# Performance work log

Hardware: AMD Instinct MI355X
Metric: run time of the kernel (lower is better)

Reference implementation:

```python
import jax, jax.numpy as jnp
import numpy as np

H = 16
HD = 128
ROPE_BASE = 10000.0

def _rope_cos_sin(T, dtype):
    inv_freq = 1.0 / (ROPE_BASE ** (jnp.arange(0, HD, 2, dtype=jnp.float32) / HD))  # [HD/2]
    pos = jnp.arange(T, dtype=jnp.float32)
    freqs = pos[:, None] * inv_freq[None, :]  # [T, HD/2]
    return jnp.cos(freqs).astype(dtype), jnp.sin(freqs).astype(dtype)

def _apply_rotary(x, cos, sin):
    # x: [B,H,T,HD]; cos/sin: [T,HD/2]
    x1, x2 = x[..., : HD // 2], x[..., HD // 2 :]
    c = cos[None, None, :, :]
    s = sin[None, None, :, :]
    return jnp.concatenate([x1 * c - x2 * s, x1 * s + x2 * c], axis=-1)

def setup_inputs() -> dict:
    key = jax.random.key(0)
    ks = jax.random.split(key, 5)
    B, T, D = 2, 2048, 2048
    x = jax.random.normal(ks[0], (B, T, D), dtype=jnp.float32)
    Wqkv = jax.random.normal(ks[1], (3 * D, D), dtype=jnp.float32) * (D ** -0.5)
    bqkv = jax.random.normal(ks[2], (3 * D,), dtype=jnp.float32) * 0.02
    Wo = jax.random.normal(ks[3], (D, D), dtype=jnp.float32) * (D ** -0.5)
    bo = jax.random.normal(ks[4], (D,), dtype=jnp.float32) * 0.02
    # causal mask: True = masked (future positions)
    mask = jnp.triu(jnp.ones((T, T), dtype=bool), k=1)[None, None, :, :]
    return {"x": x, "Wqkv": Wqkv, "bqkv": bqkv, "Wo": Wo, "bo": bo, "mask": mask}

def reference(x, Wqkv, bqkv, Wo, bo, mask):
    B, T, D = x.shape
    qkv = x @ Wqkv.T + bqkv  # [B,T,3D]
    q, k, v = jnp.split(qkv, 3, axis=-1)
    def to_heads(t):
        return t.reshape(B, T, H, HD).transpose(0, 2, 1, 3)  # [B,H,T,HD]
    q, k, v = to_heads(q), to_heads(k), to_heads(v)
    cos, sin = _rope_cos_sin(T, x.dtype)
    q = _apply_rotary(q, cos, sin)
    k = _apply_rotary(k, cos, sin)
    scale = HD ** 0.5
    attn = jnp.einsum('bhqd,bhkd->bhqk', q, k) / scale
    neg = -jnp.finfo(x.dtype).max
    attn = jnp.where(mask, neg, attn)
    w = jax.nn.softmax(attn, axis=-1)
    out = jnp.einsum('bhqk,bhkd->bhqd', w, v)  # [B,H,T,HD]
    out = out.transpose(0, 2, 1, 3).reshape(B, T, H * HD)
    return out @ Wo.T + bo
```

## Files before the change

### kernel.cpp

```cpp
#include <hip/hip_runtime.h>
#include <hip/hip_bf16.h>
#include <cstdint>

typedef __bf16 bf16;
typedef __bf16 bf16x8 __attribute__((ext_vector_type(8)));
typedef float  f32x4  __attribute__((ext_vector_type(4)));

#define B_   2
#define T_   2048
#define D_   2048
#define H_   16
#define HD_  128

typedef __attribute__((address_space(3))) void       lds_void;
typedef __attribute__((address_space(1))) const void gbl_void;
__device__ __forceinline__ void glds16(const bf16* g, bf16* l) {
    __builtin_amdgcn_global_load_lds((gbl_void*)g, (lds_void*)l, 16, 0, 0);
}

__device__ __forceinline__ ushort4 cvt4(const float4 v) {
    union { bf16 h[4]; ushort4 u; } pk;
    pk.h[0] = (bf16)v.x; pk.h[1] = (bf16)v.y;
    pk.h[2] = (bf16)v.z; pk.h[3] = (bf16)v.w;
    return pk.u;
}

__global__ __launch_bounds__(256) void convert_xw_kernel(
    const float* __restrict__ x, const float* __restrict__ wqkv,
    bf16* __restrict__ xb, bf16* __restrict__ wqkvb)
{
    const int NX = (B_ * T_ * D_) / 4;
    const int NT = NX + (3 * D_ * D_) / 4;
    for (int g = blockIdx.x * blockDim.x + threadIdx.x; g < NT;
         g += gridDim.x * blockDim.x) {
        if (g < NX) ((ushort4*)xb)[g]      = cvt4(((const float4*)x)[g]);
        else        ((ushort4*)wqkvb)[g-NX] = cvt4(((const float4*)wqkv)[g-NX]);
    }
}

__global__ __launch_bounds__(256) void convert_wo_kernel(
    const float* __restrict__ wo, bf16* __restrict__ wob)
{
    const int N = (D_ * D_) / 4;
    for (int g = blockIdx.x * blockDim.x + threadIdx.x; g < N;
         g += gridDim.x * blockDim.x)
        ((ushort4*)wob)[g] = cvt4(((const float4*)wo)[g]);
}

__device__ __forceinline__ void gemm_core_glds(
    const bf16* __restrict__ A, const bf16* __restrict__ W, int K,
    int bm, int bn, int tid, f32x4 (&acc)[4][4],
    bf16* lds_a, bf16* lds_b)
{
    const int lane = tid & 63, quad = lane >> 4, lcol = lane & 15;
    const int wave = tid >> 6;
    const int wm = (wave >> 1) * 64, wn2 = (wave & 1) * 32;
    const int sw = lcol & 7;
    const int sr = tid >> 3, pc = tid & 7;
    const int sc = (pc ^ (sr & 7)) * 8;
    const bf16* abase = A + (size_t)(bm * 128 + sr) * K + sc;
    const bf16* bbase = W + (size_t)(bn * 128 + sr) * K + sc;
    bf16* la = lds_a + sr * 64 + pc * 8;
    bf16* lb = lds_b + sr * 64 + pc * 8;

    for (int k0 = 0; k0 < K; k0 += 64) {
        __syncthreads();
#pragma unroll
        for (int p = 0; p < 4; p++) {
            glds16(abase + k0 + (size_t)32 * p * K, la + 2048 * p);
            glds16(bbase + k0 + (size_t)32 * p * K, lb + 2048 * p);
        }
        __syncthreads();
#pragma unroll
        for (int kk = 0; kk < 2; kk++) {
            bf16x8 af[4], bfr[4];
#pragma unroll
            for (int i = 0; i < 4; i++)
                af[i] = *(const bf16x8*)&lds_a[(wm + i * 16 + lcol) * 64 +
                                               (((kk * 4 + quad) ^ sw) * 8)];
#pragma unroll
            for (int j = 0; j < 4; j++) {
                const int row = wn2 + (j & 1) * 16 + (j >> 1) * 64 + lcol;
                bfr[j] = *(const bf16x8*)&lds_b[row * 64 +
                                                (((kk * 4 + quad) ^ sw) * 8)];
            }
#pragma unroll
            for (int i = 0; i < 4; i++)
#pragma unroll
                for (int j = 0; j < 4; j++)
                    acc[i][j] = __builtin_amdgcn_mfma_f32_16x16x32_bf16(af[i], bfr[j], acc[i][j], 0, 0, 0);
        }
    }
}

__global__ __launch_bounds__(512, 1) void qkv_gemm_kernel(
    const bf16* __restrict__ xb, const bf16* __restrict__ wqkvb,
    const float* __restrict__ bias,
    bf16* __restrict__ qh, bf16* __restrict__ kh, bf16* __restrict__ vT)
{
    __shared__ bf16 lds[8 * 8192];
    const int tid = threadIdx.x;
    const int bn = blockIdx.x, bm = blockIdx.y;
    const int lane = tid & 63, quad = lane >> 4, lcol = lane & 15;
    const int wave = tid >> 6;
    const int wm = wave >> 1;
    const int wn = wave & 1;
    const int swz = lcol & 7;

    const int sr = tid >> 3, sc = tid & 7;
    const bf16* ga = xb    + (size_t)(bm * 256 + sr) * D_ + ((sc ^ (sr & 7)) << 3);
    const bf16* gb = wqkvb + (size_t)(bn * 256 + sr) * D_ + ((sc ^ (sr & 7)) << 3);
    bf16* ldst = lds + tid * 8;

    auto stage = [&](int t, int kind) {
        const bf16* g = ((kind & 2) ? gb : ga) +
                        (size_t)(kind & 1) * 128 * D_ + t * 64;
        bf16* d = ldst + (((t & 1) * 4 + kind) & 7) * 8192;
        glds16(g, d);
        glds16(g + (size_t)64 * D_, d + 4096);
    };

    f32x4 acc[4][8];
    const f32x4 z = {0.f, 0.f, 0.f, 0.f};
#pragma unroll
    for (int i = 0; i < 4; i++)
#pragma unroll
        for (int j = 0; j < 8; j++) acc[i][j] = z;

    const int NT = D_ / 64;

    stage(0, 0); stage(0, 1); stage(0, 2); stage(0, 3);
    stage(1, 0); stage(1, 1);

#define QKV_TILE(t, par, LASTV)                                                \
    {                                                                          \
        if (LASTV) asm volatile("s_waitcnt vmcnt(0)" ::: "memory");            \
        else       asm volatile("s_waitcnt vmcnt(4)" ::: "memory");            \
        __builtin_amdgcn_s_barrier();                                          \
        __builtin_amdgcn_sched_barrier(0);                                     \
        if ((t) + 1 < NT) { stage((t) + 1, 2); stage((t) + 1, 3); }            \
        const bf16* sA = lds + ((par) + (wm >> 1)) * 8192 + ((wm & 1) * 64) * 64; \
        const bf16* sB = lds + ((par) + 2 + wn) * 8192;                        \
        bf16x8 af[4][2];                                                       \
        _Pragma("unroll")                                                      \
        for (int i = 0; i < 4; i++)                                            \
            _Pragma("unroll")                                                  \
            for (int kk = 0; kk < 2; kk++)                                     \
                af[i][kk] = *(const bf16x8*)&sA[(i * 16 + lcol) * 64 +         \
                                                (((kk * 4 + quad) ^ swz) << 3)]; \
        _Pragma("unroll")                                                      \
        for (int jp = 0; jp < 2; jp++) {                 \
            bf16x8 bf[2][2];                                                   \
            _Pragma("unroll")                                                  \
            for (int jj = 0; jj < 2; jj++)                                     \
                _Pragma("unroll")                                              \
                for (int kk = 0; kk < 2; kk++)                                 \
                    bf[jj][kk] = *(const bf16x8*)&sB[((jp * 2 + jj) * 16 + lcol) * 64 + \
                                                     (((kk * 4 + quad) ^ swz) << 3)]; \
            __builtin_amdgcn_s_setprio(1);                                     \
            _Pragma("unroll")                                                  \
            for (int jj = 0; jj < 2; jj++)                                     \
                _Pragma("unroll")                                              \
                for (int kk = 0; kk < 2; kk++)                                 \
                    _Pragma("unroll")                                          \
                    for (int i = 0; i < 4; i++)                                \
                        acc[i][jp * 2 + jj] = __builtin_amdgcn_mfma_f32_16x16x32_bf16( \
                            af[i][kk], bf[jj][kk], acc[i][jp * 2 + jj], 0, 0, 0); \
            __builtin_amdgcn_s_setprio(0);                                     \
        }                                                                      \
        __builtin_amdgcn_s_barrier();     \
        __builtin_amdgcn_sched_barrier(0);                                     \
        if ((t) + 2 < NT) { stage((t) + 2, 0); stage((t) + 2, 1); }            \
        _Pragma("unroll")                                                      \
        for (int jp = 2; jp < 4; jp++) {                 \
            bf16x8 bf[2][2];                                                   \
            _Pragma("unroll")                                                  \
            for (int jj = 0; jj < 2; jj++)                                     \
                _Pragma("unroll")                                              \
                for (int kk = 0; kk < 2; kk++)                                 \
                    bf[jj][kk] = *(const bf16x8*)&sB[((jp * 2 + jj) * 16 + lcol) * 64 + \
                                                     (((kk * 4 + quad) ^ swz) << 3)]; \
            __builtin_amdgcn_s_setprio(1);                                     \
            _Pragma("unroll")                                                  \
            for (int jj = 0; jj < 2; jj++)                                     \
                _Pragma("unroll")                                              \
                for (int kk = 0; kk < 2; kk++)                                 \
                    _Pragma("unroll")                                          \
                    for (int i = 0; i < 4; i++)                                \
                        acc[i][jp * 2 + jj] = __builtin_amdgcn_mfma_f32_16x16x32_bf16( \
                            af[i][kk], bf[jj][kk], acc[i][jp * 2 + jj], 0, 0, 0); \
            __builtin_amdgcn_s_setprio(0);                                     \
        }                                                                      \
    }

    for (int tt = 0; tt < 15; tt++) {
        QKV_TILE(2 * tt, 0, false);
        QKV_TILE(2 * tt + 1, 4, false);
    }
    QKV_TILE(30, 0, false);
    QKV_TILE(31, 4, true);
#undef QKV_TILE

    const int n0 = bn * 256 + wn * 128;
    const int part = bn >> 3;
    const int hh = (bn & 7) * 2 + wn;
    const int mb0 = bm * 256 + wm * 64;
    const int bb = mb0 >> 11, tb = mb0 & (T_ - 1);

    if (part < 2) {
        bf16* dst = (part == 0) ? qh : kh;
#pragma unroll
        for (int jp = 0; jp < 4; jp++) {
            const int d1 = jp * 16 + lcol;
            const float invf = __expf(-0.14391156831212787f * (float)d1);
            const float b1 = bias[n0 + d1];
            const float b2 = bias[n0 + d1 + 64];
#pragma unroll
            for (int i = 0; i < 4; i++) {
#pragma unroll
                for (int r = 0; r < 4; r++) {
                    const int t = tb + i * 16 + quad * 4 + r;
                    const float x1 = acc[i][jp][r] + b1;
                    const float x2 = acc[i][jp + 4][r] + b2;
                    float s, c;
                    __sincosf((float)t * invf, &s, &c);
                    const size_t rowo = ((size_t)(bb * H_ + hh) * T_ + t) * HD_;
                    dst[rowo + d1]      = (bf16)(x1 * c - x2 * s);
                    dst[rowo + d1 + 64] = (bf16)(x1 * s + x2 * c);
                }
            }
        }
    } else {
        const int bh = bb * H_ + hh;
#pragma unroll
        for (int j = 0; j < 8; j++) {
            const int d = j * 16 + lcol;
            const float bv = bias[n0 + d];
            bf16* vdst = &vT[((size_t)bh * HD_ + d) * T_ + tb];
#pragma unroll
            for (int r = 0; r < 4; r++) {
                union { bf16 hhv[4]; ushort4 u; } pk;
#pragma unroll
                for (int i = 0; i < 4; i++) pk.hhv[i] = (bf16)(acc[i][j][r] + bv);
                *(ushort4*)&vdst[(quad * 4 + r) * 4] = pk.u;
            }
        }
    }
}

__global__ __launch_bounds__(256) void attn_kernel(
    const bf16* __restrict__ qh, const bf16* __restrict__ kh,
    const bf16* __restrict__ vT, bf16* __restrict__ ctx)
{
    __shared__ bf16 lds_k[2][64 * 128];
    __shared__ bf16 lds_v[2][128 * 64];
    __shared__ bf16 lds_p[64 * 64];
    const int tid = threadIdx.x;
    const int id = blockIdx.x;
    const int bh = id & 31;
    const int qp = id >> 5;
    const int qtA = 31 - qp;
    const int qtB = qp;
    const int ktA = qtA + 1;
    const int lane = tid & 63, quad = lane >> 4, lcol = lane & 15;
    const int wave = tid >> 6;
    const int wq0 = wave * 16;
    const float scale2 = 0.08838834764831845f * 1.4426950408889634f;
    const int b = bh >> 4, h = bh & 15;

    const bf16* kbase = kh + (size_t)bh * T_ * HD_;
    const bf16* vbase = vT + (size_t)bh * HD_ * T_;

    const int ksrow = tid >> 4;
    const bf16* kstage = kbase + (size_t)ksrow * HD_ + (((tid & 15) ^ ksrow) << 3);
    const int vsd = tid >> 3;
    const bf16* vstage = vbase + (size_t)vsd * T_ + (((tid & 7) ^ (vsd & 7)) << 3);

    int qt_cur = qtA;
    int q0 = qtA * 64;

    bf16x8 qf[4];
    auto load_q = [&](int q0_) {
#pragma unroll
        for (int kk = 0; kk < 4; kk++)
            qf[kk] = *(const bf16x8*)&qh[((size_t)bh * T_ + q0_ + wq0 + lcol) * HD_ +
                                         kk * 32 + quad * 8];
    };
    load_q(q0);

    f32x4 o[8];
    const f32x4 z = {0.f, 0.f, 0.f, 0.f};
#pragma unroll
    for (int jd = 0; jd < 8; jd++) o[jd] = z;
    float l_part[4] = {0.f, 0.f, 0.f, 0.f};

    auto do_epilogue = [&](int q0_) {
        float inv_l[4];
#pragma unroll
        for (int r = 0; r < 4; r++) {
            float rs = l_part[r];
#pragma unroll
            for (int off = 1; off < 16; off <<= 1)
                rs += __shfl_xor(rs, off);
            inv_l[r] = 1.0f / rs;
        }
#pragma unroll
        for (int r = 0; r < 4; r++) {
            const int t = q0_ + wq0 + quad * 4 + r;
#pragma unroll
            for (int jd = 0; jd < 8; jd++)
                ctx[((size_t)(b * T_ + t)) * D_ + h * HD_ + jd * 16 + lcol] =
                    (bf16)(o[jd][r] * inv_l[r]);
        }
    };

#pragma unroll
    for (int p = 0; p < 4; p++) {
        glds16(kstage + (size_t)16 * p * HD_, &lds_k[0][tid * 8 + p * 2048]);
        glds16(vstage + (size_t)32 * p * T_, &lds_v[0][tid * 8 + p * 2048]);
    }

    for (int s = 0; s < 33; s++) {
        __syncthreads();
        if (s + 1 < 33) {
            const int kn = (s + 1 < ktA) ? (s + 1) : (s + 1 - ktA);
            const bf16* ks = kstage + (size_t)kn * 64 * HD_;
            const bf16* vs = vstage + kn * 64;
            bf16* lkd = &lds_k[(s + 1) & 1][tid * 8];
            bf16* lvd = &lds_v[(s + 1) & 1][tid * 8];
#pragma unroll
            for (int p = 0; p < 4; p++) {
                glds16(ks + (size_t)16 * p * HD_, lkd + p * 2048);
                glds16(vs + (size_t)32 * p * T_, lvd + p * 2048);
            }
        }
        if (s == ktA) {
            do_epilogue(q0);
            qt_cur = qtB;
            q0 = qtB * 64;
            load_q(q0);
#pragma unroll
            for (int jd = 0; jd < 8; jd++) o[jd] = z;
#pragma unroll
            for (int r = 0; r < 4; r++) l_part[r] = 0.f;
        }
        const int kt = (s < ktA) ? s : (s - ktA);
        const bf16* lk = lds_k[s & 1];
        const bf16* lv = lds_v[s & 1];

        f32x4 s_acc[4];
#pragma unroll
        for (int j = 0; j < 4; j++) s_acc[j] = z;
        __builtin_amdgcn_s_setprio(1);
#pragma unroll
        for (int kk = 0; kk < 4; kk++) {
#pragma unroll
            for (int j = 0; j < 4; j++) {
                const bf16x8 bk = *(const bf16x8*)&lk[(j * 16 + lcol) * 128 +
                                        (((kk * 4 + quad) ^ lcol) << 3)];
                s_acc[j] = __builtin_amdgcn_mfma_f32_16x16x32_bf16(qf[kk], bk, s_acc[j], 0, 0, 0);
            }
        }
        __builtin_amdgcn_s_setprio(0);

        const bool diag = (kt == qt_cur);
#pragma unroll
        for (int r = 0; r < 4; r++) {
            const int prow = wq0 + quad * 4 + r;
            const int qrow = q0 + prow;
            union { bf16 hh[4]; ushort4 u; } pk;
            float lp = 0.f;
#pragma unroll
            for (int j = 0; j < 4; j++) {
                float p = exp2f(fmaf(s_acc[j][r], scale2, -16.0f));
                if (diag) {
                    const int kcol = kt * 64 + j * 16 + lcol;
                    p = (kcol > qrow) ? 0.f : p;
                }
                lp += p;
                pk.hh[j] = (bf16)p;
            }
            l_part[r] += lp;
            *(ushort4*)&lds_p[prow * 64 + ((lcol * 4) ^ ((prow & 7) << 3))] = pk.u;
        }

#pragma unroll
        for (int kk2 = 0; kk2 < 2; kk2++) {
            const int prow = wq0 + lcol;
            const bf16x8 pf = *(const bf16x8*)&lds_p[prow * 64 +
                                  ((kk2 * 32 + quad * 8) ^ ((lcol & 7) << 3))];
            bf16x8 vf[8];
#pragma unroll
            for (int jd = 0; jd < 8; jd++) {
                const int d = jd * 16 + lcol;
                vf[jd] = *(const bf16x8*)&lv[d * 64 +
                              (((kk2 * 4 + quad) ^ (lcol & 7)) << 3)];
            }
            __builtin_amdgcn_s_setprio(1);
#pragma unroll
            for (int jd = 0; jd < 8; jd++)
                o[jd] = __builtin_amdgcn_mfma_f32_16x16x32_bf16(pf, vf[jd], o[jd], 0, 0, 0);
            __builtin_amdgcn_s_setprio(0);
        }
    }

    do_epilogue(q0);
}

__global__ __launch_bounds__(256) void proj_gemm_kernel(
    const bf16* __restrict__ ctx, const bf16* __restrict__ wob,
    const float* __restrict__ bias, float* __restrict__ out)
{
    __shared__ bf16 lds_a[128 * 64];
    __shared__ bf16 lds_b[128 * 64];
    const int tid = threadIdx.x;
    const int bm = blockIdx.y, bn = blockIdx.x;
    const int lane = tid & 63, quad = lane >> 4, lcol = lane & 15;
    const int wave = tid >> 6;
    const int wm = (wave >> 1) * 64, wn2 = (wave & 1) * 32;

    f32x4 acc[4][4];
    const f32x4 z = {0.f, 0.f, 0.f, 0.f};
#pragma unroll
    for (int i = 0; i < 4; i++)
#pragma unroll
        for (int j = 0; j < 4; j++) acc[i][j] = z;

    gemm_core_glds(ctx, wob, D_, bm, bn, tid, acc, lds_a, lds_b);

    const int n0 = bn * 128;
#pragma unroll
    for (int i = 0; i < 4; i++) {
#pragma unroll
        for (int j = 0; j < 4; j++) {
            const int n = n0 + wn2 + (j & 1) * 16 + (j >> 1) * 64 + lcol;
            const float bv = bias[n];
#pragma unroll
            for (int r = 0; r < 4; r++) {
                const int m = bm * 128 + wm + i * 16 + quad * 4 + r;
                out[(size_t)m * D_ + n] = acc[i][j][r] + bv;
            }
        }
    }
}

extern "C" void kernel_launch(void* const* d_in, const int* in_sizes, int n_in,
                              void* d_out, int out_size, void* d_ws, size_t ws_size,
                              hipStream_t stream)
{
    const float* x    = (const float*)d_in[0];
    const float* Wqkv = (const float*)d_in[1];
    const float* bqkv = (const float*)d_in[2];
    const float* Wo   = (const float*)d_in[3];
    const float* bo   = (const float*)d_in[4];
    float* out = (float*)d_out;

    const size_t HT = (size_t)B_ * H_ * T_ * HD_;
    bf16* xb   = (bf16*)d_ws;
    bf16* qh   = xb + HT;
    bf16* kh   = qh + HT;
    bf16* vT   = kh + HT;
    bf16* ctx  = xb;
    bf16* wob  = qh;
    bf16* wqkvb = (bf16*)d_out;

    convert_xw_kernel<<<2560, 256, 0, stream>>>(x, Wqkv, xb, wqkvb);
    qkv_gemm_kernel<<<dim3(24, 16), 512, 0, stream>>>(xb, wqkvb, bqkv, qh, kh, vT);
    attn_kernel<<<512, 256, 0, stream>>>(qh, kh, vT, ctx);
    convert_wo_kernel<<<1024, 256, 0, stream>>>(Wo, wob);
    proj_gemm_kernel<<<dim3(16, 32), 256, 0, stream>>>(ctx, wob, bo, out);
}
```

Measured before the change: 365.2 us.

## Restructure QKV GEMM main loop into four k-half phases with finer staging

The QKV projection GEMM's LDS layout now splits each 64-wide k tile into two 32-wide halves with a new XOR swizzle, and each tile is processed as four phases. Each phase loads one A/B fragment set, issues one global-to-LDS stage, and runs 16 MFMAs between barriers. The aim is to spread memory issue more evenly across compute and to reduce the register pressure of fragments. In exchange it adds more barriers per tile, and it drops the occupancy hint of 1 from launch_bounds.

```diff
diff --git a/kernel.cpp b/kernel.cpp
--- a/kernel.cpp
+++ b/kernel.cpp
@@ -93,7 +93,7 @@
     }
 }
 
-__global__ __launch_bounds__(512, 1) void qkv_gemm_kernel(
+__global__ __launch_bounds__(512) void qkv_gemm_kernel(
     const bf16* __restrict__ xb, const bf16* __restrict__ wqkvb,
     const float* __restrict__ bias,
     bf16* __restrict__ qh, bf16* __restrict__ kh, bf16* __restrict__ vT)
@@ -105,20 +105,21 @@
     const int wave = tid >> 6;
     const int wm = wave >> 1;
     const int wn = wave & 1;
-    const int swz = lcol & 7;
-
-    const int sr = tid >> 3, sc = tid & 7;
-    const bf16* ga = xb    + (size_t)(bm * 256 + sr) * D_ + ((sc ^ (sr & 7)) << 3);
-    const bf16* gb = wqkvb + (size_t)(bn * 256 + sr) * D_ + ((sc ^ (sr & 7)) << 3);
+    const int rdoff = ((quad ^ ((lcol >> 1) & 3)) << 3);
+
+    const int srow = tid >> 2, sch = tid & 3;
+    const int gsw = (sch ^ ((srow >> 1) & 3)) << 3;
+    const bf16* ga = xb    + (size_t)(bm * 256 + srow) * D_ + gsw;
+    const bf16* gb = wqkvb + (size_t)(bn * 256 + srow) * D_ + gsw;
     bf16* ldst = lds + tid * 8;
 
-    auto stage = [&](int t, int kind) {
-        const bf16* g = ((kind & 2) ? gb : ga) +
-                        (size_t)(kind & 1) * 128 * D_ + t * 64;
-        bf16* d = ldst + (((t & 1) * 4 + kind) & 7) * 8192;
-        glds16(g, d);
-        glds16(g + (size_t)64 * D_, d + 4096);
-    };
+#define STAGE(T, KIND)                                                         \
+    {                                                                          \
+        const bf16* g_ = (((KIND) & 1) ? gb : ga) + (T) * 64 + ((KIND) >> 1) * 32; \
+        bf16* d_ = ldst + (((T) & 1) * 4 + (KIND)) * 8192;                     \
+        glds16(g_, d_);                                                        \
+        glds16(g_ + (size_t)128 * D_, d_ + 4096);                              \
+    }
 
     f32x4 acc[4][8];
     const f32x4 z = {0.f, 0.f, 0.f, 0.f};
@@ -129,77 +130,65 @@
 
     const int NT = D_ / 64;
 
-    stage(0, 0); stage(0, 1); stage(0, 2); stage(0, 3);
-    stage(1, 0); stage(1, 1);
-
-#define QKV_TILE(t, par, LASTV)                                                \
+    STAGE(0, 0); STAGE(0, 1); STAGE(0, 2); STAGE(0, 3);
+    __builtin_amdgcn_sched_barrier(0);
+    asm volatile("s_waitcnt vmcnt(4)" ::: "memory");
+    __builtin_amdgcn_s_barrier();
+
+#define PHASE(PA, PB, JBASE, RD_A, T1, KIND, GUARD, LASTT)                     \
     {                                                                          \
-        if (LASTV) asm volatile("s_waitcnt vmcnt(0)" ::: "memory");            \
-        else       asm volatile("s_waitcnt vmcnt(4)" ::: "memory");            \
+        bf16x8 bfr[4];                                                         \
+        if (RD_A) {                                                            \
+            _Pragma("unroll")                                                  \
+            for (int i = 0; i < 4; i++)                                        \
+                af[i] = *(const bf16x8*)&(PA)[(wm * 64 + i * 16 + lcol) * 32 + rdoff]; \
+        }                                                                      \
+        _Pragma("unroll")                                                      \
+        for (int j = 0; j < 4; j++)                                            \
+            bfr[j] = *(const bf16x8*)&(PB)[(wn * 128 + (JBASE + j) * 16 + lcol) * 32 + rdoff]; \
+        if (!(LASTT)) STAGE(T1, KIND);                                         \
+        if (GUARD) {                                                           \
+            __builtin_amdgcn_sched_barrier(0);   \
+            if (LASTT) asm volatile("s_waitcnt vmcnt(0)" ::: "memory");        \
+            else       asm volatile("s_waitcnt vmcnt(4)" ::: "memory");        \
+        }                                                                      \
         __builtin_amdgcn_s_barrier();                                          \
+        asm volatile("s_waitcnt lgkmcnt(0)" ::: "memory");                     \
         __builtin_amdgcn_sched_barrier(0);                                     \
-        if ((t) + 1 < NT) { stage((t) + 1, 2); stage((t) + 1, 3); }            \
-        const bf16* sA = lds + ((par) + (wm >> 1)) * 8192 + ((wm & 1) * 64) * 64; \
-        const bf16* sB = lds + ((par) + 2 + wn) * 8192;                        \
-        bf16x8 af[4][2];                                                       \
+        __builtin_amdgcn_s_setprio(1);                                         \
         _Pragma("unroll")                                                      \
-        for (int i = 0; i < 4; i++)                                            \
+        for (int j = 0; j < 4; j++)                                            \
             _Pragma("unroll")                                                  \
-            for (int kk = 0; kk < 2; kk++)                                     \
-                af[i][kk] = *(const bf16x8*)&sA[(i * 16 + lcol) * 64 +         \
-                                                (((kk * 4 + quad) ^ swz) << 3)]; \
-        _Pragma("unroll")                                                      \
-        for (int jp = 0; jp < 2; jp++) {                 \
-            bf16x8 bf[2][2];                                                   \
-            _Pragma("unroll")                                                  \
-            for (int jj = 0; jj < 2; jj++)                                     \
-                _Pragma("unroll")                                              \
-                for (int kk = 0; kk < 2; kk++)                                 \
-                    bf[jj][kk] = *(const bf16x8*)&sB[((jp * 2 + jj) * 16 + lcol) * 64 + \
-                                                     (((kk * 4 + quad) ^ swz) << 3)]; \
-            __builtin_amdgcn_s_setprio(1);                                     \
-            _Pragma("unroll")                                                  \
-            for (int jj = 0; jj < 2; jj++)                                     \
-                _Pragma("unroll")                                              \
-                for (int kk = 0; kk < 2; kk++)                                 \
-                    _Pragma("unroll")                                          \
-                    for (int i = 0; i < 4; i++)                                \
-                        acc[i][jp * 2 + jj] = __builtin_amdgcn_mfma_f32_16x16x32_bf16( \
-                            af[i][kk], bf[jj][kk], acc[i][jp * 2 + jj], 0, 0, 0); \
-            __builtin_amdgcn_s_setprio(0);                                     \
-        }                                                                      \
-        __builtin_amdgcn_s_barrier();     \
+            for (int i = 0; i < 4; i++)                                        \
+                acc[i][JBASE + j] = __builtin_amdgcn_mfma_f32_16x16x32_bf16(   \
+                    af[i], bfr[j], acc[i][JBASE + j], 0, 0, 0);                \
+        __builtin_amdgcn_s_setprio(0);                                         \
         __builtin_amdgcn_sched_barrier(0);                                     \
-        if ((t) + 2 < NT) { stage((t) + 2, 0); stage((t) + 2, 1); }            \
-        _Pragma("unroll")                                                      \
-        for (int jp = 2; jp < 4; jp++) {                 \
-            bf16x8 bf[2][2];                                                   \
-            _Pragma("unroll")                                                  \
-            for (int jj = 0; jj < 2; jj++)                                     \
-                _Pragma("unroll")                                              \
-                for (int kk = 0; kk < 2; kk++)                                 \
-                    bf[jj][kk] = *(const bf16x8*)&sB[((jp * 2 + jj) * 16 + lcol) * 64 + \
-                                                     (((kk * 4 + quad) ^ swz) << 3)]; \
-            __builtin_amdgcn_s_setprio(1);                                     \
-            _Pragma("unroll")                                                  \
-            for (int jj = 0; jj < 2; jj++)                                     \
-                _Pragma("unroll")                                              \
-                for (int kk = 0; kk < 2; kk++)                                 \
-                    _Pragma("unroll")                                          \
-                    for (int i = 0; i < 4; i++)                                \
-                        acc[i][jp * 2 + jj] = __builtin_amdgcn_mfma_f32_16x16x32_bf16( \
-                            af[i][kk], bf[jj][kk], acc[i][jp * 2 + jj], 0, 0, 0); \
-            __builtin_amdgcn_s_setprio(0);                                     \
-        }                                                                      \
-    }
-
-    for (int tt = 0; tt < 15; tt++) {
-        QKV_TILE(2 * tt, 0, false);
-        QKV_TILE(2 * tt + 1, 4, false);
+        __builtin_amdgcn_s_barrier();                                         \
+    }
+
+#define QKV_TILE(T, PAR, LASTT)                                                \
+    {                                                                          \
+        const bf16* pa0 = lds + ((PAR) + 0) * 8192;                            \
+        const bf16* pb0 = lds + ((PAR) + 1) * 8192;                            \
+        const bf16* pa1 = lds + ((PAR) + 2) * 8192;                            \
+        const bf16* pb1 = lds + ((PAR) + 3) * 8192;                            \
+        bf16x8 af[4];                                                          \
+        PHASE(pa0, pb0, 0, true,  (T) + 1, 0, false, LASTT)      \
+        PHASE(pa0, pb0, 4, false, (T) + 1, 1, true,  LASTT)      \
+        PHASE(pa1, pb1, 0, true,  (T) + 1, 2, false, LASTT)      \
+        PHASE(pa1, pb1, 4, false, (T) + 1, 3, !(LASTT), LASTT)    \
+    }
+
+    for (int t2 = 0; t2 < 15; t2++) {
+        QKV_TILE(2 * t2, 0, false);
+        QKV_TILE(2 * t2 + 1, 4, false);
     }
     QKV_TILE(30, 0, false);
     QKV_TILE(31, 4, true);
 #undef QKV_TILE
+#undef PHASE
+#undef STAGE
 
     const int n0 = bn * 256 + wn * 128;
     const int part = bn >> 3;
```

New measurement: 359.5 us. About the same (-1.6%).
